# Kernel tuning notes

Hardware: AMD Instinct MI355X
Metric: run time of the kernel (lower is better)

## Reference

```python
import jax, jax.numpy as jnp
import numpy as np

BN_EPS = 1e-5

def _conv1x1(x, w, b):
    # x: [B,C,H,W], w: [O,C], b: [O] -> [B,O,H,W]
    return jnp.einsum('bchw,oc->bohw', x, w) + b[None, :, None, None]

def setup_inputs() -> dict:
    key = jax.random.key(0)
    ks = jax.random.split(key, 9)
    B, C, H, W = 8, 256, 64, 64
    I = C // 2
    s_in = 1.0 / np.sqrt(C)
    s_out = 1.0 / np.sqrt(I)
    return {
        'x':       jax.random.normal(ks[0], (B, C, H, W), dtype=jnp.float32),
        'g_w':     jax.random.uniform(ks[1], (I, C), jnp.float32, -s_in, s_in),
        'g_b':     jax.random.uniform(ks[2], (I,),  jnp.float32, -s_in, s_in),
        'theta_w': jax.random.uniform(ks[3], (I, C), jnp.float32, -s_in, s_in),
        'theta_b': jax.random.uniform(ks[4], (I,),  jnp.float32, -s_in, s_in),
        'phi_w':   jax.random.uniform(ks[5], (I, C), jnp.float32, -s_in, s_in),
        'phi_b':   jax.random.uniform(ks[6], (I,),  jnp.float32, -s_in, s_in),
        'w_w':     jax.random.uniform(ks[7], (C, I), jnp.float32, -s_out, s_out),
        'w_b':     jax.random.uniform(ks[8], (C,),  jnp.float32, -s_out, s_out),
        'gamma':   jnp.ones((C,), dtype=jnp.float32),   # BN weight init constant 1
        'beta':    jnp.zeros((C,), dtype=jnp.float32),  # BN bias init constant 0
    }

def reference(x, g_w, g_b, theta_w, theta_b, phi_w, phi_b, w_w, w_b, gamma, beta):
    B, C, H, W = x.shape
    I = g_w.shape[0]
    N = H * W
    g_x     = _conv1x1(x, g_w, g_b).reshape(B, I, N)          # [B,I,N]
    theta_x = _conv1x1(x, theta_w, theta_b).reshape(B, I, N)  # [B,I,N]
    phi_x   = _conv1x1(x, phi_w, phi_b).reshape(B, I, N)      # [B,I,N]
    # f = theta^T @ phi : [B,N,N]
    f = jnp.einsum('bin,bim->bnm', theta_x, phi_x)
    a = jax.nn.softmax(f, axis=-1)
    # y = a @ g^T : [B,N,I] -> [B,I,H,W]
    y = jnp.einsum('bnm,bim->bin', a, g_x).reshape(B, I, H, W)
    wy = _conv1x1(y, w_w, w_b)                                # [B,C,H,W]
    # BatchNorm2d (training mode: batch statistics over B,H,W per channel)
    mean = jnp.mean(wy, axis=(0, 2, 3), keepdims=True)
    var = jnp.var(wy, axis=(0, 2, 3), keepdims=True)
    wy_bn = (wy - mean) * jax.lax.rsqrt(var + BN_EPS)
    wy_bn = wy_bn * gamma[None, :, None, None] + beta[None, :, None, None]
    return wy_bn + x
```

## Files before the change

kernel.cpp:

```cpp
#include <hip/hip_runtime.h>

#define B_ 8
#define C_ 256
#define I_ 128
#define N_ 4096
#define BN_ (B_ * N_)
#define LOG2E 1.4426950408889634f

typedef __attribute__((ext_vector_type(8))) short bf16x8;
typedef __attribute__((ext_vector_type(4))) float f32x4;
typedef __attribute__((ext_vector_type(4))) int i32x4;

static __device__ __forceinline__ short f2bf(float f) {
    unsigned u = __float_as_uint(f);
    unsigned r = u + 0x7fffu + ((u >> 16) & 1u);
    return (short)(r >> 16);
}
static __device__ __forceinline__ float bf2f(short s) {
    return __uint_as_float(((unsigned)(unsigned short)s) << 16);
}
static __device__ __forceinline__ unsigned cvt_pk_bf16(float lo, float hi) {
    unsigned r;
    asm("v_cvt_pk_bf16_f32 %0, %1, %2" : "=v"(r) : "v"(lo), "v"(hi));
    return r;
}
static __device__ __forceinline__ void async_copy16(const void* g, void* l) {
    __builtin_amdgcn_global_load_lds(
        (const __attribute__((address_space(1))) void*)g,
        (__attribute__((address_space(3))) void*)l, 16, 0, 0);
}

__global__ void k_prep(const float* g_w, const float* theta_w, const float* phi_w,
                       const float* g_b, const float* theta_b, const float* phi_b,
                       const float* w_w, short* wcat, short* wwb, float* bcat,
                       float* bnsum) {
    int i = blockIdx.x * 256 + threadIdx.x;
    if (i < 384 * 256) {
        int j = i >> 8, c = i & 255;
        float v = (j < 128) ? theta_w[j * 256 + c] * LOG2E
                : (j < 256) ? phi_w[(j - 128) * 256 + c]
                            : g_w[(j - 256) * 256 + c];
        wcat[i] = f2bf(v);
    } else if (i < 384 * 256 + 256 * 128) {
        int k = i - 384 * 256;
        wwb[k] = f2bf(w_w[k]);
    } else if (i < 384 * 256 + 256 * 128 + 384) {
        int j = i - (384 * 256 + 256 * 128);
        bcat[j] = (j < 128) ? theta_b[j] * LOG2E
                : (j < 256) ? phi_b[j - 128] : g_b[j - 256];
    } else if (i < 384 * 256 + 256 * 128 + 384 + 512) {
        bnsum[i - (384 * 256 + 256 * 128 + 384)] = 0.f;
    }
}

__global__ __launch_bounds__(256) void k_proj(const float* __restrict__ x,
                                              const short* __restrict__ wcat,
                                              const float* __restrict__ bcat,
                                              short* __restrict__ tp,
                                              short* __restrict__ gmat) {
    int b = blockIdx.y;
    int n0 = blockIdx.x * 64;
    int tid = threadIdx.x;
    int wave = tid >> 6, lane = tid & 63, s = lane & 15, q = lane >> 4;
    __shared__ short xs[64][264];

#pragma unroll
    for (int it = 0; it < 16; ++it) {
        int cr = (tid >> 4) + it * 16;
        int nc = tid & 15;
        const float4 v = *(const float4*)&x[((size_t)b * C_ + cr) * N_ + n0 + nc * 4];
        xs[nc * 4 + 0][cr] = f2bf(v.x);
        xs[nc * 4 + 1][cr] = f2bf(v.y);
        xs[nc * 4 + 2][cr] = f2bf(v.z);
        xs[nc * 4 + 3][cr] = f2bf(v.w);
    }
    __syncthreads();

    f32x4 acc[4][6];
#pragma unroll
    for (int rt = 0; rt < 4; ++rt)
#pragma unroll
        for (int jt = 0; jt < 6; ++jt) acc[rt][jt] = (f32x4){0.f, 0.f, 0.f, 0.f};

#pragma unroll
    for (int kb = 0; kb < 8; ++kb) {
        bf16x8 af[4], bfv[6];
#pragma unroll
        for (int rt = 0; rt < 4; ++rt)
            af[rt] = *(const bf16x8*)&xs[rt * 16 + s][kb * 32 + q * 8];
#pragma unroll
        for (int jt = 0; jt < 6; ++jt)
            bfv[jt] = *(const bf16x8*)&wcat[(wave * 96 + jt * 16 + s) * 256 + kb * 32 + q * 8];
#pragma unroll
        for (int rt = 0; rt < 4; ++rt)
#pragma unroll
            for (int jt = 0; jt < 6; ++jt)
                acc[rt][jt] = __builtin_amdgcn_mfma_f32_16x16x32_bf16(af[rt], bfv[jt], acc[rt][jt], 0, 0, 0);
    }

#pragma unroll
    for (int rt = 0; rt < 4; ++rt)
#pragma unroll
        for (int jt = 0; jt < 6; ++jt) {
            int j = wave * 96 + jt * 16 + s;
            float bias = bcat[j];
#pragma unroll
            for (int r = 0; r < 4; ++r) {
                int n = n0 + rt * 16 + 4 * q + r;
                float v = acc[rt][jt][r] + bias;
                if (j < 256)
                    tp[((size_t)b * N_ + n) * 256 + j] = f2bf(v);
                else
                    gmat[((size_t)b * I_ + (j - 256)) * N_ + n] = f2bf(v);
            }
        }
}

__global__ __launch_bounds__(512, 2) void k_attn_wy(const short* __restrict__ tp,
                                                    const short* __restrict__ gmat,
                                                    const short* __restrict__ wwb,
                                                    const float* __restrict__ w_b,
                                                    short* __restrict__ wyh,
                                                    float* __restrict__ bnsum) {
    int id = blockIdx.x;
    int b = id & 7;
    int qt = id >> 3;
    int n0 = qt * 128;
    int tid = threadIdx.x;
    int wave = tid >> 6, lane = tid & 63, s = lane & 15, q = lane >> 4;
    int kg = wave >> 2, qg = wave & 3;

    __shared__ __align__(16) short SH[65536];
    __shared__ float l_lds[2][128];
    char* base = (char*)SH;

    const int swz = (s & 7) << 4;
    int kA[4];
#pragma unroll
    for (int kb = 0; kb < 4; ++kb) kA[kb] = s * 256 + ((kb * 64 + q * 16) ^ swz);
    int vA[2];
#pragma unroll
    for (int kb2 = 0; kb2 < 2; ++kb2) vA[kb2] = s * 256 + ((kb2 * 64 + q * 16) ^ swz);

    int rl = lane >> 4;
    int colS = ((lane & 15) * 16) ^ ((((wave & 1) << 2) | rl) << 4);
    const char* gK = (const char*)tp + ((size_t)b * N_ + wave * 4 + rl) * 512 + 256 + colS;
    const char* gV = (const char*)gmat + ((size_t)b * I_ + wave * 4 + rl) * 8192 + colS;
    const int ldsSt = wave * 1024;

    i32x4 onesw = (i32x4){0x3F803F80, 0x3F803F80, 0x3F803F80, 0x3F803F80};
    bf16x8 vone = __builtin_bit_cast(bf16x8, onesw);

    bf16x8 qf[2][4];
#pragma unroll
    for (int fr = 0; fr < 2; ++fr) {
        const short* qb = tp + ((size_t)b * N_ + n0 + qg * 32 + fr * 16 + s) * 256;
#pragma unroll
        for (int kb = 0; kb < 4; ++kb) qf[fr][kb] = *(const bf16x8*)(qb + kb * 32 + q * 8);
    }

    f32x4 ot[2][8];
#pragma unroll
    for (int fr = 0; fr < 2; ++fr)
#pragma unroll
        for (int t = 0; t < 8; ++t) ot[fr][t] = (f32x4){0.f, 0.f, 0.f, 0.f};
    f32x4 lacc[2] = {(f32x4){0.f, 0.f, 0.f, 0.f}, (f32x4){0.f, 0.f, 0.f, 0.f}};

#pragma unroll
    for (int it = 0; it < 4; ++it) {
        async_copy16(gK + it * 16384, base + ldsSt + it * 8192);
        async_copy16(gV + it * 262144, base + 32768 + ldsSt + it * 8192);
    }
    __syncthreads();

    const int hK = kg * 16384, hV = kg * 128;

    for (int i = 0; i < 32; ++i) {
        char* KtB = base + (i & 1) * 65536;
        char* VtB = KtB + 32768;
        if (i < 31) {
            char* Kd = base + (((i & 1) ^ 1) * 65536) + ldsSt;
            size_t m = (size_t)(i + 1) * 128;
#pragma unroll
            for (int it = 0; it < 4; ++it) {
                async_copy16(gK + m * 512 + it * 16384, Kd + it * 8192);
                async_copy16(gV + m * 2 + it * 262144, Kd + 32768 + it * 8192);
            }
        }

        f32x4 sa[2][4];
#pragma unroll
        for (int fr = 0; fr < 2; ++fr)
#pragma unroll
            for (int tc = 0; tc < 4; ++tc) sa[fr][tc] = (f32x4){0.f, 0.f, 0.f, 0.f};
        __builtin_amdgcn_s_setprio(1);
#pragma unroll
        for (int tc = 0; tc < 4; ++tc) {
            bf16x8 bfv[4];
#pragma unroll
            for (int kb = 0; kb < 4; ++kb)
                bfv[kb] = *(const bf16x8*)(KtB + hK + kA[kb] + tc * 4096);
#pragma unroll
            for (int fr = 0; fr < 2; ++fr)
#pragma unroll
                for (int kb = 0; kb < 4; ++kb)
                    sa[fr][tc] = __builtin_amdgcn_mfma_f32_16x16x32_bf16(bfv[kb], qf[fr][kb], sa[fr][tc], 0, 0, 0);
        }
        __builtin_amdgcn_s_setprio(0);

        unsigned W[2][4][2];
#pragma unroll
        for (int fr = 0; fr < 2; ++fr) {
#pragma unroll
            for (int tc = 0; tc < 4; ++tc)
#pragma unroll
                for (int r = 0; r < 4; ++r) sa[fr][tc][r] = exp2f(sa[fr][tc][r]);
#pragma unroll
            for (int tc = 0; tc < 4; ++tc) {
                W[fr][tc][0] = cvt_pk_bf16(sa[fr][tc][0], sa[fr][tc][1]);
                W[fr][tc][1] = cvt_pk_bf16(sa[fr][tc][2], sa[fr][tc][3]);
            }
        }

#pragma unroll
        for (int kb2 = 0; kb2 < 2; ++kb2) {
            bf16x8 pa[2];
#pragma unroll
            for (int fr = 0; fr < 2; ++fr) {
                unsigned rA = W[fr][2 * kb2 + 0][0];
                unsigned rB = W[fr][2 * kb2 + 0][1];
                unsigned rC = W[fr][2 * kb2 + 1][0];
                unsigned rD = W[fr][2 * kb2 + 1][1];
                asm("v_permlane32_swap_b32 %0, %1" : "+v"(rA), "+v"(rC));
                asm("v_permlane32_swap_b32 %0, %1" : "+v"(rB), "+v"(rD));
                asm("v_permlane16_swap_b32 %0, %1" : "+v"(rA), "+v"(rC));
                asm("v_permlane16_swap_b32 %0, %1" : "+v"(rB), "+v"(rD));
                i32x4 wv = (i32x4){(int)rA, (int)rB, (int)rC, (int)rD};
                pa[fr] = __builtin_bit_cast(bf16x8, wv);
            }
            __builtin_amdgcn_s_setprio(1);
            lacc[0] = __builtin_amdgcn_mfma_f32_16x16x32_bf16(pa[0], vone, lacc[0], 0, 0, 0);
            lacc[1] = __builtin_amdgcn_mfma_f32_16x16x32_bf16(pa[1], vone, lacc[1], 0, 0, 0);
#pragma unroll
            for (int t = 0; t < 8; ++t) {
                bf16x8 vb = *(const bf16x8*)(VtB + hV + vA[kb2] + t * 4096);
                ot[0][t] = __builtin_amdgcn_mfma_f32_16x16x32_bf16(pa[0], vb, ot[0][t], 0, 0, 0);
                ot[1][t] = __builtin_amdgcn_mfma_f32_16x16x32_bf16(pa[1], vb, ot[1][t], 0, 0, 0);
            }
            __builtin_amdgcn_s_setprio(0);
        }
        __syncthreads();
    }

    if (s == 0) {
#pragma unroll
        for (int fr = 0; fr < 2; ++fr)
#pragma unroll
            for (int r = 0; r < 4; ++r)
                l_lds[kg][qg * 32 + fr * 16 + 4 * q + r] = lacc[fr][r];
    }
    if (kg == 1) {
#pragma unroll
        for (int fr = 0; fr < 2; ++fr)
#pragma unroll
            for (int t = 0; t < 8; ++t)
#pragma unroll
                for (int r = 0; r < 4; ++r) {
                    int row = qg * 32 + fr * 16 + 4 * q + r;
                    int colb = (t * 16 + s) * 4;
                    *(float*)(base + row * 512 + (colb ^ ((row & 7) << 4))) = ot[fr][t][r];
                }
    }
    __syncthreads();
    if (kg == 0) {
#pragma unroll
        for (int fr = 0; fr < 2; ++fr)
#pragma unroll
            for (int t = 0; t < 8; ++t)
#pragma unroll
                for (int r = 0; r < 4; ++r) {
                    int row = qg * 32 + fr * 16 + 4 * q + r;
                    int colb = (t * 16 + s) * 4;
                    float p = *(const float*)(base + row * 512 + (colb ^ ((row & 7) << 4)));
                    float v = ot[fr][t][r] + p;
                    int byt = 65536 + row * 256 + (((t * 16 + s) * 2) ^ ((row & 7) << 4));
                    *(short*)(base + byt) = f2bf(v);
                }
    }
    __syncthreads();

    f32x4 acc[2][8];
#pragma unroll
    for (int ct = 0; ct < 2; ++ct)
#pragma unroll
        for (int jt = 0; jt < 8; ++jt) acc[ct][jt] = (f32x4){0.f, 0.f, 0.f, 0.f};
#pragma unroll
    for (int kb = 0; kb < 4; ++kb) {
        bf16x8 af[2];
#pragma unroll
        for (int ct = 0; ct < 2; ++ct)
            af[ct] = *(const bf16x8*)&wwb[(wave * 32 + ct * 16 + s) * 128 + kb * 32 + q * 8];
#pragma unroll
        for (int jt = 0; jt < 8; ++jt) {
            bf16x8 yb = *(const bf16x8*)(base + 65536 + kA[kb] + jt * 4096);
#pragma unroll
            for (int ct = 0; ct < 2; ++ct)
                acc[ct][jt] = __builtin_amdgcn_mfma_f32_16x16x32_bf16(af[ct], yb, acc[ct][jt], 0, 0, 0);
        }
    }
    float linv[8];
#pragma unroll
    for (int jt = 0; jt < 8; ++jt)
        linv[jt] = 1.0f / (l_lds[0][jt * 16 + s] + l_lds[1][jt * 16 + s]);
#pragma unroll
    for (int ct = 0; ct < 2; ++ct)
#pragma unroll
        for (int r = 0; r < 4; ++r) {
            int c = wave * 32 + ct * 16 + 4 * q + r;
            float bias = w_b[c];
            float s1 = 0.f, s2 = 0.f;
#pragma unroll
            for (int jt = 0; jt < 8; ++jt) {
                float v = acc[ct][jt][r] * linv[jt] + bias;
                short w = f2bf(v);
                wyh[((size_t)b * C_ + c) * N_ + n0 + jt * 16 + s] = w;
                float vr = bf2f(w);
                s1 += vr;
                s2 += vr * vr;
            }
#pragma unroll
            for (int off = 1; off < 16; off <<= 1) {
                s1 += __shfl_xor(s1, off);
                s2 += __shfl_xor(s2, off);
            }
            if (s == 0) {
                atomicAdd(&bnsum[c], s1);
                atomicAdd(&bnsum[256 + c], s2);
            }
        }
}

__global__ __launch_bounds__(256) void k_out(const short* __restrict__ wyh,
                                             const float* __restrict__ x,
                                             const float* __restrict__ bnsum,
                                             const float* __restrict__ gamma,
                                             const float* __restrict__ beta,
                                             float* __restrict__ out) {
    int gid = blockIdx.x * 256 + threadIdx.x;
    size_t base = (size_t)gid * 8;
    int c = (int)((base >> 12) & 255);
    const float inv = 1.0f / 32768.0f;
    float mean = bnsum[c] * inv;
    float var = bnsum[256 + c] * inv - mean * mean;
    float sc = gamma[c] * rsqrtf(var + 1e-5f);
    float sh = beta[c] - mean * sc;
    bf16x8 w = *(const bf16x8*)&wyh[base];
    float4 x0 = *(const float4*)&x[base];
    float4 x1 = *(const float4*)&x[base + 4];
    float4 o0, o1;
    o0.x = bf2f(w[0]) * sc + sh + x0.x;
    o0.y = bf2f(w[1]) * sc + sh + x0.y;
    o0.z = bf2f(w[2]) * sc + sh + x0.z;
    o0.w = bf2f(w[3]) * sc + sh + x0.w;
    o1.x = bf2f(w[4]) * sc + sh + x1.x;
    o1.y = bf2f(w[5]) * sc + sh + x1.y;
    o1.z = bf2f(w[6]) * sc + sh + x1.z;
    o1.w = bf2f(w[7]) * sc + sh + x1.w;
    *(float4*)&out[base] = o0;
    *(float4*)&out[base + 4] = o1;
}

extern "C" void kernel_launch(void* const* d_in, const int* in_sizes, int n_in,
                              void* d_out, int out_size, void* d_ws, size_t ws_size,
                              hipStream_t stream) {
    const float* x       = (const float*)d_in[0];
    const float* g_w     = (const float*)d_in[1];
    const float* g_b     = (const float*)d_in[2];
    const float* theta_w = (const float*)d_in[3];
    const float* theta_b = (const float*)d_in[4];
    const float* phi_w   = (const float*)d_in[5];
    const float* phi_b   = (const float*)d_in[6];
    const float* w_w     = (const float*)d_in[7];
    const float* w_b     = (const float*)d_in[8];
    const float* gamma   = (const float*)d_in[9];
    const float* beta    = (const float*)d_in[10];

    char* ws = (char*)d_ws;
    size_t off = 0;
    auto alloc = [&](size_t bytes) {
        void* p = ws + off;
        off += (bytes + 255) & ~(size_t)255;
        return p;
    };
    short*  wcat  = (short*)alloc((size_t)384 * 256 * 2);
    short*  wwb   = (short*)alloc((size_t)256 * 128 * 2);
    float*  bcat  = (float*)alloc((size_t)384 * 4);
    float*  bnsum = (float*)alloc(512 * 4);
    short*  tp    = (short*)alloc((size_t)BN_ * 256 * 2);
    short*  gmat  = (short*)alloc((size_t)B_ * I_ * N_ * 2);
    short*  wyh   = (short*)alloc((size_t)BN_ * C_ * 2);

    k_prep<<<516, 256, 0, stream>>>(g_w, theta_w, phi_w, g_b, theta_b, phi_b, w_w,
                                    wcat, wwb, bcat, bnsum);
    k_proj<<<dim3(64, 8), 256, 0, stream>>>(x, wcat, bcat, tp, gmat);
    k_attn_wy<<<256, 512, 0, stream>>>(tp, gmat, wwb, w_b, wyh, bnsum);
    k_out<<<4096, 256, 0, stream>>>(wyh, x, bnsum, gamma, beta, (float*)d_out);
}
```

Baseline: 252.6 us.

## Split attention keys across four wave groups with 1024-thread blocks

The attention kernel goes from 512 to 1024 threads, so each key tile is split four ways across wave groups instead of two. Partial outputs are combined with a two-stage reduction through LDS. K/V staging now uses register prefetch plus LDS stores instead of async global-to-LDS copies. The PV product uses 16x16x16 MFMA on the exp tile directly, which removes the permlane shuffles, and the row sum is done with VALU adds instead of an MFMA against a ones vector. The extra waves are meant to raise occupancy and hide latency, at the cost of more barriers, more reduction traffic and tighter register limits.

```diff
diff --git a/kernel.cpp b/kernel.cpp
--- a/kernel.cpp
+++ b/kernel.cpp
@@ -9,7 +9,7 @@
 
 typedef __attribute__((ext_vector_type(8))) short bf16x8;
 typedef __attribute__((ext_vector_type(4))) float f32x4;
-typedef __attribute__((ext_vector_type(4))) int i32x4;
+typedef __attribute__((ext_vector_type(2))) int i32x2;
 
 static __device__ __forceinline__ short f2bf(float f) {
     unsigned u = __float_as_uint(f);
@@ -24,10 +24,9 @@
     asm("v_cvt_pk_bf16_f32 %0, %1, %2" : "=v"(r) : "v"(lo), "v"(hi));
     return r;
 }
-static __device__ __forceinline__ void async_copy16(const void* g, void* l) {
-    __builtin_amdgcn_global_load_lds(
-        (const __attribute__((address_space(1))) void*)g,
-        (__attribute__((address_space(3))) void*)l, 16, 0, 0);
+static __device__ __forceinline__ f32x4 mfma16(i32x2 a, i32x2 b, f32x4 c) {
+    asm("v_mfma_f32_16x16x16_bf16 %0, %1, %2, %0" : "+v"(c) : "v"(a), "v"(b));
+    return c;
 }
 
 __global__ void k_prep(const float* g_w, const float* theta_w, const float* phi_w,
@@ -116,40 +115,31 @@
         }
 }
 
-__global__ __launch_bounds__(512, 2) void k_attn_wy(const short* __restrict__ tp,
-                                                    const short* __restrict__ gmat,
-                                                    const short* __restrict__ wwb,
-                                                    const float* __restrict__ w_b,
-                                                    short* __restrict__ wyh,
-                                                    float* __restrict__ bnsum) {
+__global__ __launch_bounds__(1024, 4) void k_attn_wy(const short* __restrict__ tp,
+                                                     const short* __restrict__ gmat,
+                                                     const short* __restrict__ wwb,
+                                                     const float* __restrict__ w_b,
+                                                     short* __restrict__ wyh,
+                                                     float* __restrict__ bnsum) {
     int id = blockIdx.x;
     int b = id & 7;
     int qt = id >> 3;
     int n0 = qt * 128;
     int tid = threadIdx.x;
     int wave = tid >> 6, lane = tid & 63, s = lane & 15, q = lane >> 4;
-    int kg = wave >> 2, qg = wave & 3;
+    int qg = wave & 3, kg = wave >> 2;
 
     __shared__ __align__(16) short SH[65536];
-    __shared__ float l_lds[2][128];
+    __shared__ float l_lds[4][128];
     char* base = (char*)SH;
 
     const int swz = (s & 7) << 4;
     int kA[4];
 #pragma unroll
     for (int kb = 0; kb < 4; ++kb) kA[kb] = s * 256 + ((kb * 64 + q * 16) ^ swz);
-    int vA[2];
-#pragma unroll
-    for (int kb2 = 0; kb2 < 2; ++kb2) vA[kb2] = s * 256 + ((kb2 * 64 + q * 16) ^ swz);
-
-    int rl = lane >> 4;
-    int colS = ((lane & 15) * 16) ^ ((((wave & 1) << 2) | rl) << 4);
-    const char* gK = (const char*)tp + ((size_t)b * N_ + wave * 4 + rl) * 512 + 256 + colS;
-    const char* gV = (const char*)gmat + ((size_t)b * I_ + wave * 4 + rl) * 8192 + colS;
-    const int ldsSt = wave * 1024;
-
-    i32x4 onesw = (i32x4){0x3F803F80, 0x3F803F80, 0x3F803F80, 0x3F803F80};
-    bf16x8 vone = __builtin_bit_cast(bf16x8, onesw);
+
+    int krow = tid >> 4, kch = tid & 15;
+    int stW = krow * 256 + ((kch * 16) ^ ((krow & 7) << 4));
 
     bf16x8 qf[2][4];
 #pragma unroll
@@ -164,42 +154,48 @@
     for (int fr = 0; fr < 2; ++fr)
 #pragma unroll
         for (int t = 0; t < 8; ++t) ot[fr][t] = (f32x4){0.f, 0.f, 0.f, 0.f};
-    f32x4 lacc[2] = {(f32x4){0.f, 0.f, 0.f, 0.f}, (f32x4){0.f, 0.f, 0.f, 0.f}};
-
-#pragma unroll
-    for (int it = 0; it < 4; ++it) {
-        async_copy16(gK + it * 16384, base + ldsSt + it * 8192);
-        async_copy16(gV + it * 262144, base + 32768 + ldsSt + it * 8192);
-    }
-    __syncthreads();
-
-    const int hK = kg * 16384, hV = kg * 128;
+    float lsum[2] = {0.f, 0.f};
+
+    bf16x8 pk[2], pv[2];
+#pragma unroll
+    for (int it = 0; it < 2; ++it) {
+        pk[it] = *(const bf16x8*)&tp[((size_t)b * N_ + krow + it * 64) * 256 + 128 + kch * 8];
+        pv[it] = *(const bf16x8*)&gmat[((size_t)b * I_ + krow + it * 64) * N_ + kch * 8];
+    }
+#pragma unroll
+    for (int it = 0; it < 2; ++it) {
+        *(bf16x8*)(base + stW + it * 16384) = pk[it];
+        *(bf16x8*)(base + 32768 + stW + it * 16384) = pv[it];
+    }
+    __syncthreads();
+
+    const int kgK = kg * 8192;
+    const int kgV = kg * 64;
 
     for (int i = 0; i < 32; ++i) {
         char* KtB = base + (i & 1) * 65536;
         char* VtB = KtB + 32768;
         if (i < 31) {
-            char* Kd = base + (((i & 1) ^ 1) * 65536) + ldsSt;
             size_t m = (size_t)(i + 1) * 128;
 #pragma unroll
-            for (int it = 0; it < 4; ++it) {
-                async_copy16(gK + m * 512 + it * 16384, Kd + it * 8192);
-                async_copy16(gV + m * 2 + it * 262144, Kd + 32768 + it * 8192);
-            }
-        }
-
-        f32x4 sa[2][4];
-#pragma unroll
-        for (int fr = 0; fr < 2; ++fr)
-#pragma unroll
-            for (int tc = 0; tc < 4; ++tc) sa[fr][tc] = (f32x4){0.f, 0.f, 0.f, 0.f};
+            for (int it = 0; it < 2; ++it) {
+                pk[it] = *(const bf16x8*)&tp[((size_t)b * N_ + m + krow + it * 64) * 256 + 128 + kch * 8];
+                pv[it] = *(const bf16x8*)&gmat[((size_t)b * I_ + krow + it * 64) * N_ + m + kch * 8];
+            }
+        }
+
+        f32x4 sa[2][2];
+#pragma unroll
+        for (int fr = 0; fr < 2; ++fr)
+#pragma unroll
+            for (int tc = 0; tc < 2; ++tc) sa[fr][tc] = (f32x4){0.f, 0.f, 0.f, 0.f};
         __builtin_amdgcn_s_setprio(1);
 #pragma unroll
-        for (int tc = 0; tc < 4; ++tc) {
+        for (int tc = 0; tc < 2; ++tc) {
             bf16x8 bfv[4];
 #pragma unroll
             for (int kb = 0; kb < 4; ++kb)
-                bfv[kb] = *(const bf16x8*)(KtB + hK + kA[kb] + tc * 4096);
+                bfv[kb] = *(const bf16x8*)(KtB + kgK + tc * 4096 + kA[kb]);
 #pragma unroll
             for (int fr = 0; fr < 2; ++fr)
 #pragma unroll
@@ -208,58 +204,102 @@
         }
         __builtin_amdgcn_s_setprio(0);
 
-        unsigned W[2][4][2];
+        unsigned Wp[2][2][2];
 #pragma unroll
         for (int fr = 0; fr < 2; ++fr) {
 #pragma unroll
-            for (int tc = 0; tc < 4; ++tc)
+            for (int tc = 0; tc < 2; ++tc)
 #pragma unroll
                 for (int r = 0; r < 4; ++r) sa[fr][tc][r] = exp2f(sa[fr][tc][r]);
-#pragma unroll
-            for (int tc = 0; tc < 4; ++tc) {
-                W[fr][tc][0] = cvt_pk_bf16(sa[fr][tc][0], sa[fr][tc][1]);
-                W[fr][tc][1] = cvt_pk_bf16(sa[fr][tc][2], sa[fr][tc][3]);
-            }
-        }
-
-#pragma unroll
-        for (int kb2 = 0; kb2 < 2; ++kb2) {
-            bf16x8 pa[2];
-#pragma unroll
-            for (int fr = 0; fr < 2; ++fr) {
-                unsigned rA = W[fr][2 * kb2 + 0][0];
-                unsigned rB = W[fr][2 * kb2 + 0][1];
-                unsigned rC = W[fr][2 * kb2 + 1][0];
-                unsigned rD = W[fr][2 * kb2 + 1][1];
-                asm("v_permlane32_swap_b32 %0, %1" : "+v"(rA), "+v"(rC));
-                asm("v_permlane32_swap_b32 %0, %1" : "+v"(rB), "+v"(rD));
-                asm("v_permlane16_swap_b32 %0, %1" : "+v"(rA), "+v"(rC));
-                asm("v_permlane16_swap_b32 %0, %1" : "+v"(rB), "+v"(rD));
-                i32x4 wv = (i32x4){(int)rA, (int)rB, (int)rC, (int)rD};
-                pa[fr] = __builtin_bit_cast(bf16x8, wv);
-            }
-            __builtin_amdgcn_s_setprio(1);
-            lacc[0] = __builtin_amdgcn_mfma_f32_16x16x32_bf16(pa[0], vone, lacc[0], 0, 0, 0);
-            lacc[1] = __builtin_amdgcn_mfma_f32_16x16x32_bf16(pa[1], vone, lacc[1], 0, 0, 0);
+            lsum[fr] += ((sa[fr][0][0] + sa[fr][0][1]) + (sa[fr][0][2] + sa[fr][0][3]))
+                      + ((sa[fr][1][0] + sa[fr][1][1]) + (sa[fr][1][2] + sa[fr][1][3]));
+#pragma unroll
+            for (int tc = 0; tc < 2; ++tc) {
+                Wp[fr][tc][0] = cvt_pk_bf16(sa[fr][tc][0], sa[fr][tc][1]);
+                Wp[fr][tc][1] = cvt_pk_bf16(sa[fr][tc][2], sa[fr][tc][3]);
+            }
+        }
+
+        __builtin_amdgcn_s_setprio(1);
+#pragma unroll
+        for (int tc = 0; tc < 2; ++tc) {
+            i32x2 pa0 = (i32x2){(int)Wp[0][tc][0], (int)Wp[0][tc][1]};
+            i32x2 pa1 = (i32x2){(int)Wp[1][tc][0], (int)Wp[1][tc][1]};
 #pragma unroll
             for (int t = 0; t < 8; ++t) {
-                bf16x8 vb = *(const bf16x8*)(VtB + hV + vA[kb2] + t * 4096);
-                ot[0][t] = __builtin_amdgcn_mfma_f32_16x16x32_bf16(pa[0], vb, ot[0][t], 0, 0, 0);
-                ot[1][t] = __builtin_amdgcn_mfma_f32_16x16x32_bf16(pa[1], vb, ot[1][t], 0, 0, 0);
-            }
-            __builtin_amdgcn_s_setprio(0);
+                i32x2 vb = *(const i32x2*)(VtB + (t * 16 + s) * 256 + ((kgV + tc * 32 + q * 8) ^ swz));
+                ot[0][t] = mfma16(pa0, vb, ot[0][t]);
+                ot[1][t] = mfma16(pa1, vb, ot[1][t]);
+            }
+        }
+        __builtin_amdgcn_s_setprio(0);
+
+        if (i < 31) {
+            char* KtN = base + ((i & 1) ^ 1) * 65536;
+#pragma unroll
+            for (int it = 0; it < 2; ++it) {
+                *(bf16x8*)(KtN + stW + it * 16384) = pk[it];
+                *(bf16x8*)(KtN + 32768 + stW + it * 16384) = pv[it];
+            }
         }
         __syncthreads();
     }
 
-    if (s == 0) {
-#pragma unroll
-        for (int fr = 0; fr < 2; ++fr)
-#pragma unroll
-            for (int r = 0; r < 4; ++r)
-                l_lds[kg][qg * 32 + fr * 16 + 4 * q + r] = lacc[fr][r];
-    }
-    if (kg == 1) {
+#pragma unroll
+    for (int fr = 0; fr < 2; ++fr) {
+        lsum[fr] += __shfl_xor(lsum[fr], 16);
+        lsum[fr] += __shfl_xor(lsum[fr], 32);
+    }
+    if (q == 0) {
+#pragma unroll
+        for (int fr = 0; fr < 2; ++fr) l_lds[kg][qg * 32 + fr * 16 + s] = lsum[fr];
+    }
+
+#define O_ADDR(D, i_, rb_) ((D) + (i_) * 512 + ((rb_) ^ (((i_) & 7) << 4)))
+    if (kg == 1 || kg == 3) {
+        char* D = base + (kg == 3 ? 65536 : 0);
+#pragma unroll
+        for (int fr = 0; fr < 2; ++fr)
+#pragma unroll
+            for (int t = 0; t < 8; ++t) {
+                int ii = t * 16 + s;
+                int rb = (qg * 32 + fr * 16 + 4 * q) * 4;
+                *(f32x4*)O_ADDR(D, ii, rb) = ot[fr][t];
+            }
+    }
+    __syncthreads();
+    if (kg == 0 || kg == 2) {
+        const char* D = base + (kg == 2 ? 65536 : 0);
+#pragma unroll
+        for (int fr = 0; fr < 2; ++fr)
+#pragma unroll
+            for (int t = 0; t < 8; ++t) {
+                int ii = t * 16 + s;
+                int rb = (qg * 32 + fr * 16 + 4 * q) * 4;
+                ot[fr][t] += *(const f32x4*)O_ADDR(D, ii, rb);
+            }
+    }
+    __syncthreads();
+    if (kg == 2) {
+#pragma unroll
+        for (int fr = 0; fr < 2; ++fr)
+#pragma unroll
+            for (int t = 0; t < 8; ++t) {
+                int ii = t * 16 + s;
+                int rb = (qg * 32 + fr * 16 + 4 * q) * 4;
+                *(f32x4*)O_ADDR(base, ii, rb) = ot[fr][t];
+            }
+    }
+    __syncthreads();
+    if (kg == 0) {
+#pragma unroll
+        for (int fr = 0; fr < 2; ++fr)
+#pragma unroll
+            for (int t = 0; t < 8; ++t) {
+                int ii = t * 16 + s;
+                int rb = (qg * 32 + fr * 16 + 4 * q) * 4;
+                ot[fr][t] += *(const f32x4*)O_ADDR(base, ii, rb);
+            }
 #pragma unroll
         for (int fr = 0; fr < 2; ++fr)
 #pragma unroll
@@ -267,77 +307,55 @@
 #pragma unroll
                 for (int r = 0; r < 4; ++r) {
                     int row = qg * 32 + fr * 16 + 4 * q + r;
-                    int colb = (t * 16 + s) * 4;
-                    *(float*)(base + row * 512 + (colb ^ ((row & 7) << 4))) = ot[fr][t][r];
+                    int byt = 65536 + row * 256 + (((t * 16 + s) * 2) ^ ((row & 7) << 4));
+                    *(short*)(base + byt) = f2bf(ot[fr][t][r]);
                 }
     }
     __syncthreads();
-    if (kg == 0) {
-#pragma unroll
-        for (int fr = 0; fr < 2; ++fr)
-#pragma unroll
-            for (int t = 0; t < 8; ++t)
-#pragma unroll
-                for (int r = 0; r < 4; ++r) {
-                    int row = qg * 32 + fr * 16 + 4 * q + r;
-                    int colb = (t * 16 + s) * 4;
-                    float p = *(const float*)(base + row * 512 + (colb ^ ((row & 7) << 4)));
-                    float v = ot[fr][t][r] + p;
-                    int byt = 65536 + row * 256 + (((t * 16 + s) * 2) ^ ((row & 7) << 4));
-                    *(short*)(base + byt) = f2bf(v);
-                }
-    }
-    __syncthreads();
-
-    f32x4 acc[2][8];
-#pragma unroll
-    for (int ct = 0; ct < 2; ++ct)
-#pragma unroll
-        for (int jt = 0; jt < 8; ++jt) acc[ct][jt] = (f32x4){0.f, 0.f, 0.f, 0.f};
+#undef O_ADDR
+
+    f32x4 acc[8];
+#pragma unroll
+    for (int jt = 0; jt < 8; ++jt) acc[jt] = (f32x4){0.f, 0.f, 0.f, 0.f};
 #pragma unroll
     for (int kb = 0; kb < 4; ++kb) {
-        bf16x8 af[2];
-#pragma unroll
-        for (int ct = 0; ct < 2; ++ct)
-            af[ct] = *(const bf16x8*)&wwb[(wave * 32 + ct * 16 + s) * 128 + kb * 32 + q * 8];
+        bf16x8 af = *(const bf16x8*)&wwb[(wave * 16 + s) * 128 + kb * 32 + q * 8];
 #pragma unroll
         for (int jt = 0; jt < 8; ++jt) {
-            bf16x8 yb = *(const bf16x8*)(base + 65536 + kA[kb] + jt * 4096);
-#pragma unroll
-            for (int ct = 0; ct < 2; ++ct)
-                acc[ct][jt] = __builtin_amdgcn_mfma_f32_16x16x32_bf16(af[ct], yb, acc[ct][jt], 0, 0, 0);
+            bf16x8 yb = *(const bf16x8*)(base + 65536 + (jt * 16 + s) * 256 + ((kb * 64 + q * 16) ^ swz));
+            acc[jt] = __builtin_amdgcn_mfma_f32_16x16x32_bf16(af, yb, acc[jt], 0, 0, 0);
         }
     }
     float linv[8];
 #pragma unroll
-    for (int jt = 0; jt < 8; ++jt)
-        linv[jt] = 1.0f / (l_lds[0][jt * 16 + s] + l_lds[1][jt * 16 + s]);
-#pragma unroll
-    for (int ct = 0; ct < 2; ++ct)
-#pragma unroll
-        for (int r = 0; r < 4; ++r) {
-            int c = wave * 32 + ct * 16 + 4 * q + r;
-            float bias = w_b[c];
-            float s1 = 0.f, s2 = 0.f;
-#pragma unroll
-            for (int jt = 0; jt < 8; ++jt) {
-                float v = acc[ct][jt][r] * linv[jt] + bias;
-                short w = f2bf(v);
-                wyh[((size_t)b * C_ + c) * N_ + n0 + jt * 16 + s] = w;
-                float vr = bf2f(w);
-                s1 += vr;
-                s2 += vr * vr;
-            }
-#pragma unroll
-            for (int off = 1; off < 16; off <<= 1) {
-                s1 += __shfl_xor(s1, off);
-                s2 += __shfl_xor(s2, off);
-            }
-            if (s == 0) {
-                atomicAdd(&bnsum[c], s1);
-                atomicAdd(&bnsum[256 + c], s2);
-            }
-        }
+    for (int jt = 0; jt < 8; ++jt) {
+        int nl = jt * 16 + s;
+        linv[jt] = 1.0f / (((l_lds[0][nl] + l_lds[1][nl]) + (l_lds[2][nl] + l_lds[3][nl])));
+    }
+#pragma unroll
+    for (int r = 0; r < 4; ++r) {
+        int c = wave * 16 + 4 * q + r;
+        float bias = w_b[c];
+        float s1 = 0.f, s2 = 0.f;
+#pragma unroll
+        for (int jt = 0; jt < 8; ++jt) {
+            float v = acc[jt][r] * linv[jt] + bias;
+            short w = f2bf(v);
+            wyh[((size_t)b * C_ + c) * N_ + n0 + jt * 16 + s] = w;
+            float vr = bf2f(w);
+            s1 += vr;
+            s2 += vr * vr;
+        }
+#pragma unroll
+        for (int off = 1; off < 16; off <<= 1) {
+            s1 += __shfl_xor(s1, off);
+            s2 += __shfl_xor(s2, off);
+        }
+        if (s == 0) {
+            atomicAdd(&bnsum[c], s1);
+            atomicAdd(&bnsum[256 + c], s2);
+        }
+    }
 }
 
 __global__ __launch_bounds__(256) void k_out(const short* __restrict__ wyh,
@@ -403,6 +421,6 @@
     k_prep<<<516, 256, 0, stream>>>(g_w, theta_w, phi_w, g_b, theta_b, phi_b, w_w,
                                     wcat, wwb, bcat, bnsum);
     k_proj<<<dim3(64, 8), 256, 0, stream>>>(x, wcat, bcat, tp, gmat);
-    k_attn_wy<<<256, 512, 0, stream>>>(tp, gmat, wwb, w_b, wyh, bnsum);
+    k_attn_wy<<<256, 1024, 0, stream>>>(tp, gmat, wwb, w_b, wyh, bnsum);
     k_out<<<4096, 256, 0, stream>>>(wyh, x, bnsum, gamma, beta, (float*)d_out);
 }
```

Result: slower. 531.6 us (+110.5%).

## Stage projection outputs through LDS and prefetch K/V via registers

Applied to the files above, without the earlier changes.

The projection kernel now writes its tp and gmat outputs into a shared-memory tile first, then stores them to global memory as contiguous 16-byte vectors instead of scattered 2-byte stores. In the attention kernel, the direct global-to-LDS async copies are replaced by register prefetch: the next K/V tile is loaded into registers at the start of each iteration and written to the swizzled LDS buffer after the compute. This aims at coalesced writes and overlap of global loads with MFMA work. The cost is extra registers and extra LDS write instructions, which could lower occupancy under the 512-thread, 2-block launch bound.

```diff
diff --git a/kernel.cpp b/kernel.cpp
--- a/kernel.cpp
+++ b/kernel.cpp
@@ -23,11 +23,6 @@
     unsigned r;
     asm("v_cvt_pk_bf16_f32 %0, %1, %2" : "=v"(r) : "v"(lo), "v"(hi));
     return r;
-}
-static __device__ __forceinline__ void async_copy16(const void* g, void* l) {
-    __builtin_amdgcn_global_load_lds(
-        (const __attribute__((address_space(1))) void*)g,
-        (__attribute__((address_space(3))) void*)l, 16, 0, 0);
 }
 
 __global__ void k_prep(const float* g_w, const float* theta_w, const float* phi_w,
@@ -62,7 +57,8 @@
     int n0 = blockIdx.x * 64;
     int tid = threadIdx.x;
     int wave = tid >> 6, lane = tid & 63, s = lane & 15, q = lane >> 4;
-    __shared__ short xs[64][264];
+    __shared__ __align__(16) char SM[33024];
+    short (*xs)[258] = (short(*)[258])SM;
 
 #pragma unroll
     for (int it = 0; it < 16; ++it) {
@@ -97,23 +93,54 @@
             for (int jt = 0; jt < 6; ++jt)
                 acc[rt][jt] = __builtin_amdgcn_mfma_f32_16x16x32_bf16(af[rt], bfv[jt], acc[rt][jt], 0, 0, 0);
     }
-
-#pragma unroll
-    for (int rt = 0; rt < 4; ++rt)
-#pragma unroll
-        for (int jt = 0; jt < 6; ++jt) {
-            int j = wave * 96 + jt * 16 + s;
+    __syncthreads();
+
+    short* ytile = (short*)SM;
+#pragma unroll
+    for (int jt = 0; jt < 6; ++jt) {
+        int j = wave * 96 + jt * 16 + s;
+        if (j < 256) {
             float bias = bcat[j];
 #pragma unroll
-            for (int r = 0; r < 4; ++r) {
-                int n = n0 + rt * 16 + 4 * q + r;
-                float v = acc[rt][jt][r] + bias;
-                if (j < 256)
-                    tp[((size_t)b * N_ + n) * 256 + j] = f2bf(v);
-                else
-                    gmat[((size_t)b * I_ + (j - 256)) * N_ + n] = f2bf(v);
-            }
-        }
+            for (int rt = 0; rt < 4; ++rt)
+#pragma unroll
+                for (int r = 0; r < 4; ++r)
+                    ytile[(rt * 16 + 4 * q + r) * 256 + j] = f2bf(acc[rt][jt][r] + bias);
+        }
+    }
+    __syncthreads();
+    {
+        short* dst = tp + ((size_t)b * N_ + n0) * 256;
+#pragma unroll
+        for (int k = 0; k < 8; ++k) {
+            int off = k * 2048 + tid * 8;
+            *(bf16x8*)(dst + off) = *(const bf16x8*)(ytile + off);
+        }
+    }
+    __syncthreads();
+
+    short* gt = (short*)SM;
+#pragma unroll
+    for (int jt = 0; jt < 6; ++jt) {
+        int j = wave * 96 + jt * 16 + s;
+        if (j >= 256) {
+            float bias = bcat[j];
+            int i2 = j - 256;
+#pragma unroll
+            for (int rt = 0; rt < 4; ++rt)
+#pragma unroll
+                for (int r = 0; r < 4; ++r)
+                    gt[i2 * 66 + rt * 16 + 4 * q + r] = f2bf(acc[rt][jt][r] + bias);
+        }
+    }
+    __syncthreads();
+#pragma unroll
+    for (int k = 0; k < 4; ++k) {
+        int idx = k * 256 + tid;
+        int i2 = idx >> 3, nch = idx & 7;
+        bf16x8 v = *(const bf16x8*)(gt + i2 * 66 + nch * 8);
+        *(bf16x8*)&gmat[((size_t)b * I_ + i2) * N_ + n0 + nch * 8] = v;
+    }
 }
 
 __global__ __launch_bounds__(512, 2) void k_attn_wy(const short* __restrict__ tp,
@@ -141,12 +168,8 @@
     int vA[2];
 #pragma unroll
     for (int kb2 = 0; kb2 < 2; ++kb2) vA[kb2] = s * 256 + ((kb2 * 64 + q * 16) ^ swz);
-
-    int rl = lane >> 4;
-    int colS = ((lane & 15) * 16) ^ ((((wave & 1) << 2) | rl) << 4);
-    const char* gK = (const char*)tp + ((size_t)b * N_ + wave * 4 + rl) * 512 + 256 + colS;
-    const char* gV = (const char*)gmat + ((size_t)b * I_ + wave * 4 + rl) * 8192 + colS;
-    const int ldsSt = wave * 1024;
+    int krow = tid >> 4, kch = tid & 15;
+    int stW = krow * 256 + ((kch * 16) ^ ((krow & 7) << 4));
 
     i32x4 onesw = (i32x4){0x3F803F80, 0x3F803F80, 0x3F803F80, 0x3F803F80};
     bf16x8 vone = __builtin_bit_cast(bf16x8, onesw);
@@ -166,10 +189,16 @@
         for (int t = 0; t < 8; ++t) ot[fr][t] = (f32x4){0.f, 0.f, 0.f, 0.f};
     f32x4 lacc[2] = {(f32x4){0.f, 0.f, 0.f, 0.f}, (f32x4){0.f, 0.f, 0.f, 0.f}};
 
+    bf16x8 pk[4], pv[4];
 #pragma unroll
     for (int it = 0; it < 4; ++it) {
-        async_copy16(gK + it * 16384, base + ldsSt + it * 8192);
-        async_copy16(gV + it * 262144, base + 32768 + ldsSt + it * 8192);
+        pk[it] = *(const bf16x8*)&tp[((size_t)b * N_ + krow + it * 32) * 256 + 128 + kch * 8];
+        pv[it] = *(const bf16x8*)&gmat[((size_t)b * I_ + krow + it * 32) * N_ + kch * 8];
+    }
+#pragma unroll
+    for (int it = 0; it < 4; ++it) {
+        *(bf16x8*)(base + stW + it * 8192) = pk[it];
+        *(bf16x8*)(base + 32768 + stW + it * 8192) = pv[it];
     }
     __syncthreads();
 
@@ -179,12 +208,11 @@
         char* KtB = base + (i & 1) * 65536;
         char* VtB = KtB + 32768;
         if (i < 31) {
-            char* Kd = base + (((i & 1) ^ 1) * 65536) + ldsSt;
             size_t m = (size_t)(i + 1) * 128;
 #pragma unroll
             for (int it = 0; it < 4; ++it) {
-                async_copy16(gK + m * 512 + it * 16384, Kd + it * 8192);
-                async_copy16(gV + m * 2 + it * 262144, Kd + 32768 + it * 8192);
+                pk[it] = *(const bf16x8*)&tp[((size_t)b * N_ + m + krow + it * 32) * 256 + 128 + kch * 8];
+                pv[it] = *(const bf16x8*)&gmat[((size_t)b * I_ + krow + it * 32) * N_ + m + kch * 8];
             }
         }
 
@@ -248,6 +276,15 @@
                 ot[1][t] = __builtin_amdgcn_mfma_f32_16x16x32_bf16(pa[1], vb, ot[1][t], 0, 0, 0);
             }
             __builtin_amdgcn_s_setprio(0);
+        }
+
+        if (i < 31) {
+            char* KtN = base + ((i & 1) ^ 1) * 65536;
+#pragma unroll
+            for (int it = 0; it < 4; ++it) {
+                *(bf16x8*)(KtN + stW + it * 8192) = pk[it];
+                *(bf16x8*)(KtN + 32768 + stW + it * 8192) = pv[it];
+            }
         }
         __syncthreads();
     }
```

Result: faster. 244.9 us (-3.1%).
